# Kernel tuning notes

Measured on AMD Instinct MI355X. Metric: run time of the kernel, lower is better.

Reference implementation:

```python
import jax, jax.numpy as jnp
import numpy as np

B, T, C, H = 8, 1024, 1024, 16
Dh = C // H
EPS = 1e-5


def layernorm(x, g, b):
    m = jnp.mean(x, axis=-1, keepdims=True)
    v = jnp.mean((x - m) ** 2, axis=-1, keepdims=True)
    return g * (x - m) / jnp.sqrt(v + EPS) + b


def setup_inputs() -> dict:
    key = jax.random.key(0)
    ks = jax.random.split(key, 10)
    s = 0.02
    return {
        "x": jax.random.normal(ks[0], (B, T, C), jnp.float32),
        "Wq": jax.random.normal(ks[1], (H, C, Dh), jnp.float32) * s,
        "Wk": jax.random.normal(ks[2], (H, C, Dh), jnp.float32) * s,
        "Wv": jax.random.normal(ks[3], (H, C, Dh), jnp.float32) * s,
        "Wproj": jax.random.normal(ks[4], (C, C), jnp.float32) * s,
        "bproj": jnp.zeros((C,), jnp.float32),
        "W1": jax.random.normal(ks[5], (C, C), jnp.float32) * s,
        "b1": jnp.zeros((C,), jnp.float32),
        "W2": jax.random.normal(ks[6], (C, C), jnp.float32) * s,
        "b2": jnp.zeros((C,), jnp.float32),
        "g1": jnp.ones((C,), jnp.float32),
        "beta1": jnp.zeros((C,), jnp.float32),
        "g2": jnp.ones((C,), jnp.float32),
        "beta2": jnp.zeros((C,), jnp.float32),
    }


def reference(x, Wq, Wk, Wv, Wproj, bproj, W1, b1, W2, b2, g1, beta1, g2, beta2):
    # pre-LN multi-head causal self-attention + residual
    xn = layernorm(x, g1, beta1)
    q = jnp.einsum("btc,hcd->bhtd", xn, Wq)
    k = jnp.einsum("btc,hcd->bhtd", xn, Wk)
    v = jnp.einsum("btc,hcd->bhtd", xn, Wv)
    scores = jnp.einsum("bhtd,bhsd->bhts", q, k) * (Dh ** -0.5)
    causal = jnp.tril(jnp.ones((T, T), bool))  # [T,T]
    scores = jnp.where(causal, scores, -jnp.inf)
    wei = jax.nn.softmax(scores, axis=-1)
    attn = jnp.einsum("bhts,bhsd->bhtd", wei, v)
    attn = attn.transpose(0, 2, 1, 3).reshape(B, T, C)  # concat heads
    x = x + attn @ Wproj + bproj
    # pre-LN MLP (n_emb -> n_emb, ReLU, n_emb -> n_emb) + residual
    xn2 = layernorm(x, g2, beta2)
    h = jax.nn.relu(xn2 @ W1 + b1)
    x = x + h @ W2 + b2
    return x
```

## Files before the change

### kernel.cpp

```cpp
#include <hip/hip_runtime.h>
#include <hip/hip_bf16.h>

#define KDIM 1024

typedef __bf16  bf16x8  __attribute__((ext_vector_type(8)));
typedef float   floatx4 __attribute__((ext_vector_type(4)));

__device__ inline short f2bf(float f) {
    unsigned u = __float_as_uint(f);
    u += 0x7fffu + ((u >> 16) & 1u);
    return (short)(u >> 16);
}

__device__ inline floatx4 mfma16(bf16x8 a, bf16x8 b, floatx4 c) {
    return __builtin_amdgcn_mfma_f32_16x16x32_bf16(a, b, c, 0, 0, 0);
}

__device__ inline void load_lds16(const void* g, void* l) {
    __builtin_amdgcn_global_load_lds(
        (__attribute__((address_space(1))) void*)(unsigned long long)g,
        (__attribute__((address_space(3))) void*)(unsigned)(unsigned long long)l,
        16, 0, 0);
}

__global__ __launch_bounds__(256) void ln_kernel(
    const float* __restrict__ x, const float* __restrict__ g,
    const float* __restrict__ be, short* __restrict__ out)
{
    const int row = blockIdx.x, tid = threadIdx.x;
    const float4 v = ((const float4*)(x + (size_t)row * 1024))[tid];
    float s  = v.x + v.y + v.z + v.w;
    float s2 = v.x * v.x + v.y * v.y + v.z * v.z + v.w * v.w;
    #pragma unroll
    for (int off = 32; off; off >>= 1) {
        s  += __shfl_down(s, off);
        s2 += __shfl_down(s2, off);
    }
    __shared__ float red1[4], red2[4];
    const int w = tid >> 6, lane = tid & 63;
    if (lane == 0) { red1[w] = s; red2[w] = s2; }
    __syncthreads();
    s  = red1[0] + red1[1] + red1[2] + red1[3];
    s2 = red2[0] + red2[1] + red2[2] + red2[3];
    const float mean = s * (1.0f / 1024.0f);
    const float var  = s2 * (1.0f / 1024.0f) - mean * mean;
    const float rstd = rsqrtf(var + 1e-5f);
    const float4 gg = ((const float4*)g)[tid];
    const float4 bb = ((const float4*)be)[tid];
    short4 o;
    o.x = f2bf((v.x - mean) * rstd * gg.x + bb.x);
    o.y = f2bf((v.y - mean) * rstd * gg.y + bb.y);
    o.z = f2bf((v.z - mean) * rstd * gg.z + bb.z);
    o.w = f2bf((v.w - mean) * rstd * gg.w + bb.w);
    *(short4*)(out + (size_t)row * 1024 + tid * 4) = o;
}

__global__ void pack_qkvT(const float* __restrict__ Wq, const float* __restrict__ Wk,
                          const float* __restrict__ Wv, short* __restrict__ dst)
{
    __shared__ float tile[32][33];
    const int n0 = blockIdx.x * 32, c0 = blockIdx.y * 32;
    const int tx = threadIdx.x, ty = threadIdx.y;
    const int grp = n0 >> 10;
    const float* W = (grp == 0) ? Wq : (grp == 1 ? Wk : Wv);
    const int nb = n0 & 1023, hh = nb >> 6, d0 = nb & 63;
    #pragma unroll
    for (int j = 0; j < 32; j += 8)
        tile[ty + j][tx] = W[hh * 65536 + (c0 + ty + j) * 64 + d0 + tx];
    __syncthreads();
    #pragma unroll
    for (int j = 0; j < 32; j += 8)
        dst[(size_t)(n0 + ty + j) * 1024 + c0 + tx] = f2bf(tile[tx][ty + j]);
}

__global__ void packT(const float* __restrict__ src, short* __restrict__ dst)
{
    __shared__ float tile[32][33];
    const int n0 = blockIdx.x * 32, k0 = blockIdx.y * 32;
    const int tx = threadIdx.x, ty = threadIdx.y;
    #pragma unroll
    for (int j = 0; j < 32; j += 8)
        tile[ty + j][tx] = src[(size_t)(k0 + ty + j) * 1024 + n0 + tx];
    __syncthreads();
    #pragma unroll
    for (int j = 0; j < 32; j += 8)
        dst[(size_t)(n0 + ty + j) * 1024 + k0 + tx] = f2bf(tile[tx][ty + j]);
}

template <int EPI, bool SWAP>
__global__ __launch_bounds__(256) void gemm_bt(
    const short* __restrict__ A, const short* __restrict__ BT, int N,
    const float* __restrict__ bias, const float* __restrict__ resid,
    float* __restrict__ outF, short* __restrict__ outH,
    short* __restrict__ qO, short* __restrict__ kO, short* __restrict__ vtO)
{
    const int tid = threadIdx.x, lane = tid & 63, w = tid >> 6;
    const int wm = w >> 1, wn = w & 1;
    const int mi = lane & 15, quad = lane >> 4;
    const int rowBase = blockIdx.y * 128, colBase = blockIdx.x * 128;

    __shared__ alignas(16) short As[128 * 32];
    __shared__ alignas(16) short Bs[128 * 32];

    const floatx4 z4 = {0.f, 0.f, 0.f, 0.f};
    floatx4 acc[4][4];
    #pragma unroll
    for (int i = 0; i < 4; ++i)
        #pragma unroll
        for (int j = 0; j < 4; ++j) acc[i][j] = z4;

    for (int k0 = 0; k0 < KDIM; k0 += 32) {
        __syncthreads();
        #pragma unroll
        for (int i = 0; i < 2; ++i) {
            const int cb = i * 256 + w * 64;
            const int chunk = cb + lane;
            const int r = chunk >> 2, cc = chunk & 3;
            const int csw = cc ^ ((r >> 1) & 3);
            load_lds16(A  + (size_t)(rowBase + r) * KDIM + k0 + csw * 8, (char*)As + cb * 16);
            load_lds16(BT + (size_t)(colBase + r) * KDIM + k0 + csw * 8, (char*)Bs + cb * 16);
        }
        __syncthreads();
        bf16x8 af[4], bfv[4];
        #pragma unroll
        for (int it = 0; it < 4; ++it) {
            const int ra = wm * 64 + it * 16 + mi;
            af[it] = *(const bf16x8*)(As + ra * 32 + ((quad ^ ((ra >> 1) & 3)) << 3));
        }
        #pragma unroll
        for (int jt = 0; jt < 4; ++jt) {
            const int rb = wn * 64 + jt * 16 + mi;
            bfv[jt] = *(const bf16x8*)(Bs + rb * 32 + ((quad ^ ((rb >> 1) & 3)) << 3));
        }
        #pragma unroll
        for (int it = 0; it < 4; ++it)
            #pragma unroll
            for (int jt = 0; jt < 4; ++jt) {
                if constexpr (SWAP)
                    acc[it][jt] = mfma16(bfv[jt], af[it], acc[it][jt]);
                else
                    acc[it][jt] = mfma16(af[it], bfv[jt], acc[it][jt]);
            }
    }

    if constexpr (SWAP) {
        #pragma unroll
        for (int it = 0; it < 4; ++it) {
            const int row = rowBase + wm * 64 + it * 16 + mi;
            #pragma unroll
            for (int jt = 0; jt < 4; ++jt) {
                const int col0 = colBase + wn * 64 + jt * 16 + quad * 4;
                const floatx4 a4 = acc[it][jt];
                if constexpr (EPI == 0) {
                    if (colBase < 1024) {
                        short4 o;
                        o.x = f2bf(a4[0] * 0.125f); o.y = f2bf(a4[1] * 0.125f);
                        o.z = f2bf(a4[2] * 0.125f); o.w = f2bf(a4[3] * 0.125f);
                        *(short4*)(qO + (size_t)row * 1024 + col0) = o;
                    } else {
                        short4 o;
                        o.x = f2bf(a4[0]); o.y = f2bf(a4[1]);
                        o.z = f2bf(a4[2]); o.w = f2bf(a4[3]);
                        *(short4*)(kO + (size_t)row * 1024 + (col0 - 1024)) = o;
                    }
                } else if constexpr (EPI == 1) {
                    const float4 b4 = *(const float4*)(bias + col0);
                    const float4 r4 = *(const float4*)(resid + (size_t)row * N + col0);
                    float4 o;
                    o.x = a4[0] + b4.x + r4.x; o.y = a4[1] + b4.y + r4.y;
                    o.z = a4[2] + b4.z + r4.z; o.w = a4[3] + b4.w + r4.w;
                    *(float4*)(outF + (size_t)row * N + col0) = o;
                } else {
                    const float4 b4 = *(const float4*)(bias + col0);
                    short4 o;
                    o.x = f2bf(fmaxf(a4[0] + b4.x, 0.f));
                    o.y = f2bf(fmaxf(a4[1] + b4.y, 0.f));
                    o.z = f2bf(fmaxf(a4[2] + b4.z, 0.f));
                    o.w = f2bf(fmaxf(a4[3] + b4.w, 0.f));
                    *(short4*)(outH + (size_t)row * N + col0) = o;
                }
            }
        }
    } else {
        #pragma unroll
        for (int it = 0; it < 4; ++it) {
            const int row0 = rowBase + wm * 64 + it * 16 + quad * 4;
            const int bb = row0 >> 10, t0 = row0 & 1023;
            #pragma unroll
            for (int jt = 0; jt < 4; ++jt) {
                const int c = colBase + wn * 64 + jt * 16 + mi;
                const floatx4 a4 = acc[it][jt];
                short4 o;
                o.x = f2bf(a4[0]); o.y = f2bf(a4[1]);
                o.z = f2bf(a4[2]); o.w = f2bf(a4[3]);
                *(short4*)(vtO + ((size_t)bb << 20) + ((size_t)c << 10) + t0) = o;
            }
        }
    }
}

#define PSTR 88
__device__ __forceinline__ void attn_qk_pv(
    const bf16x8 qf0, const bf16x8 qf1,
    floatx4 (&o)[4], float (&lsum)[4],
    const short* Ks, const short* Vs, short* myP,
    const int mi, const int quad, const int kq, const int diagRowOff)
{
    const floatx4 z4 = {0.f, 0.f, 0.f, 0.f};
    const bool diag = diagRowOff >= 0;
    floatx4 sa[4];
    #pragma unroll
    for (int j = 0; j < 4; ++j) {
        const int row = j * 16 + mi;
        const int sw = row & 7;
        floatx4 s4 = z4;
        s4 = mfma16(qf0, *(const bf16x8*)(Ks + row * 64 + ((quad ^ sw) << 3)), s4);
        s4 = mfma16(qf1, *(const bf16x8*)(Ks + row * 64 + (((quad + 4) ^ sw) << 3)), s4);
        sa[j] = s4;
    }
    #pragma unroll
    for (int j = 0; j < 4; ++j)
        #pragma unroll
        for (int r = 0; r < 4; ++r) {
            float p = __expf(sa[j][r]);
            if (diag && (j * 16 + mi > diagRowOff + quad * 4 + r)) p = 0.f;
            lsum[r] += p;
            myP[(quad * 4 + r) * PSTR + j * 16 + mi] = f2bf(p);
        }
    __asm__ volatile("s_waitcnt lgkmcnt(0)" ::: "memory");
    const bf16x8 pf0 = *(const bf16x8*)(myP + mi * PSTR + kq);
    const bf16x8 pf1 = *(const bf16x8*)(myP + mi * PSTR + 32 + kq);
    #pragma unroll
    for (int d = 0; d < 4; ++d) {
        const int row = d * 16 + mi;
        const int sw = row & 7;
        o[d] = mfma16(pf0, *(const bf16x8*)(Vs + row * 64 + ((quad ^ sw) << 3)), o[d]);
        o[d] = mfma16(pf1, *(const bf16x8*)(Vs + row * 64 + (((quad + 4) ^ sw) << 3)), o[d]);
    }
}

__global__ __launch_bounds__(256, 4) void flash_attn(
    const short* __restrict__ Q, const short* __restrict__ K,
    const short* __restrict__ Vt, short* __restrict__ O)
{
    const int tid = threadIdx.x, lane = tid & 63, w = tid >> 6;
    const int mi = lane & 15, quad = lane >> 4, kq = quad * 8;
    const int pi = blockIdx.x;
    const int tA = pi, tB = 15 - pi;
    const int h = blockIdx.y, b = blockIdx.z;
    const int qbA = tA * 64, qbB = tB * 64;

    __shared__ alignas(16) short Ks[64 * 64];
    __shared__ alignas(16) short Vs[64 * 64];
    __shared__ alignas(16) short Ps[4][16 * PSTR];

    const size_t qoffA = ((size_t)(b * 1024 + qbA + w * 16 + mi)) * 1024 + h * 64;
    const size_t qoffB = ((size_t)(b * 1024 + qbB + w * 16 + mi)) * 1024 + h * 64;
    const bf16x8 qA0 = *(const bf16x8*)(Q + qoffA + kq);
    const bf16x8 qA1 = *(const bf16x8*)(Q + qoffA + 32 + kq);
    const bf16x8 qB0 = *(const bf16x8*)(Q + qoffB + kq);
    const bf16x8 qB1 = *(const bf16x8*)(Q + qoffB + 32 + kq);

    const floatx4 z4 = {0.f, 0.f, 0.f, 0.f};
    floatx4 oA[4], oB[4];
    float lA[4], lB[4];
    #pragma unroll
    for (int i = 0; i < 4; ++i) { oA[i] = z4; oB[i] = z4; lA[i] = 0.f; lB[i] = 0.f; }

    short* myP = &Ps[w][0];
    for (int t = 0; t <= tB; ++t) {
        const int s0 = t * 64;
        __syncthreads();
        #pragma unroll
        for (int i = 0; i < 2; ++i) {
            const int cb = i * 256 + w * 64;
            const int chunk = cb + lane;
            const int r = chunk >> 3, c = chunk & 7;
            const int csw = c ^ (r & 7);
            load_lds16(K + ((size_t)(b * 1024 + s0 + r)) * 1024 + h * 64 + csw * 8,
                       (char*)Ks + cb * 16);
            load_lds16(Vt + ((size_t)b << 20) + ((size_t)(h * 64 + r) << 10) + s0 + csw * 8,
                       (char*)Vs + cb * 16);
        }
        __syncthreads();

        if (t <= tA)
            attn_qk_pv(qA0, qA1, oA, lA, Ks, Vs, myP, mi, quad, kq,
                       (t == tA) ? (w * 16) : -1);
        attn_qk_pv(qB0, qB1, oB, lB, Ks, Vs, myP, mi, quad, kq,
                   (t == tB) ? (w * 16) : -1);
    }

    #pragma unroll
    for (int r = 0; r < 4; ++r) {
        float sA = lA[r], sB = lB[r];
        #pragma unroll
        for (int off = 1; off < 16; off <<= 1) {
            sA += __shfl_xor(sA, off);
            sB += __shfl_xor(sB, off);
        }
        lA[r] = 1.0f / sA;
        lB[r] = 1.0f / sB;
    }
    #pragma unroll
    for (int d = 0; d < 4; ++d)
        #pragma unroll
        for (int r = 0; r < 4; ++r) {
            const int col = h * 64 + d * 16 + mi;
            const int rowA = b * 1024 + qbA + w * 16 + quad * 4 + r;
            const int rowB = b * 1024 + qbB + w * 16 + quad * 4 + r;
            O[(size_t)rowA * 1024 + col] = f2bf(oA[d][r] * lA[r]);
            O[(size_t)rowB * 1024 + col] = f2bf(oB[d][r] * lB[r]);
        }
}

extern "C" void kernel_launch(void* const* d_in, const int* in_sizes, int n_in,
                              void* d_out, int out_size, void* d_ws, size_t ws_size,
                              hipStream_t stream)
{
    (void)in_sizes; (void)n_in; (void)out_size; (void)ws_size;
    const float* x     = (const float*)d_in[0];
    const float* Wq    = (const float*)d_in[1];
    const float* Wk    = (const float*)d_in[2];
    const float* Wv    = (const float*)d_in[3];
    const float* Wproj = (const float*)d_in[4];
    const float* bproj = (const float*)d_in[5];
    const float* W1    = (const float*)d_in[6];
    const float* b1    = (const float*)d_in[7];
    const float* W2    = (const float*)d_in[8];
    const float* b2    = (const float*)d_in[9];
    const float* g1    = (const float*)d_in[10];
    const float* be1   = (const float*)d_in[11];
    const float* g2    = (const float*)d_in[12];
    const float* be2   = (const float*)d_in[13];
    float* out = (float*)d_out;

    char* ws = (char*)d_ws;
    const size_t MB = 1u << 20;
    short* Qb     = (short*)(ws + 0 * MB);
    short* Kb     = (short*)(ws + 16 * MB);
    short* Vtb    = (short*)(ws + 32 * MB);
    short* XN     = (short*)(ws + 48 * MB);
    short* AT     = (short*)(ws + 64 * MB);
    float* R2     = (float*)(ws + 80 * MB);
    short* WqkvT  = (short*)(ws + 112 * MB);
    short* WprojT = (short*)(ws + 118 * MB);
    short* W1T    = (short*)(ws + 120 * MB);
    short* W2T    = (short*)(ws + 122 * MB);

    const dim3 tb(32, 8);
    pack_qkvT<<<dim3(96, 32), tb, 0, stream>>>(Wq, Wk, Wv, WqkvT);
    packT<<<dim3(32, 32), tb, 0, stream>>>(Wproj, WprojT);
    packT<<<dim3(32, 32), tb, 0, stream>>>(W1, W1T);
    packT<<<dim3(32, 32), tb, 0, stream>>>(W2, W2T);

    ln_kernel<<<8192, 256, 0, stream>>>(x, g1, be1, XN);

    gemm_bt<0, true><<<dim3(16, 64), 256, 0, stream>>>(XN, WqkvT, 1024,
        nullptr, nullptr, nullptr, nullptr, Qb, Kb, nullptr);
    gemm_bt<3, false><<<dim3(8, 64), 256, 0, stream>>>(XN, WqkvT + 2048 * KDIM, 1024,
        nullptr, nullptr, nullptr, nullptr, nullptr, nullptr, Vtb);

    flash_attn<<<dim3(8, 16, 8), 256, 0, stream>>>(Qb, Kb, Vtb, AT);

    gemm_bt<1, true><<<dim3(8, 64), 256, 0, stream>>>(AT, WprojT, 1024,
        bproj, x, R2, nullptr, nullptr, nullptr, nullptr);

    ln_kernel<<<8192, 256, 0, stream>>>(R2, g2, be2, XN);

    gemm_bt<2, true><<<dim3(8, 64), 256, 0, stream>>>(XN, W1T, 1024,
        b1, nullptr, nullptr, AT, nullptr, nullptr, nullptr);

    gemm_bt<1, true><<<dim3(8, 64), 256, 0, stream>>>(AT, W2T, 1024,
        b2, R2, out, nullptr, nullptr, nullptr, nullptr);
}
```

Before: 373.1 us.

## Deepen GEMM K-tile to 64, remap blocks per XCD, store residual in bf16

The GEMM main loop now stages 64-wide K slices with an 8-way XOR swizzle and runs two MFMA sub-steps per barrier pair, which halves the number of synchronisations. GEMM and flash-attention block indices are remapped so that neighbouring row tiles or heads land on the same XCD, aiming for better L2 reuse. The post-attention residual is written as bf16 instead of fp32, which cuts traffic for the second LayerNorm and the final residual add. The cost is doubled LDS per GEMM block and lower precision in the residual stream.

```diff
diff --git a/kernel.cpp b/kernel.cpp
--- a/kernel.cpp
+++ b/kernel.cpp
@@ -10,6 +10,9 @@
     unsigned u = __float_as_uint(f);
     u += 0x7fffu + ((u >> 16) & 1u);
     return (short)(u >> 16);
+}
+__device__ inline float bf2f(short s) {
+    return __uint_as_float(((unsigned)(unsigned short)s) << 16);
 }
 
 __device__ inline floatx4 mfma16(bf16x8 a, bf16x8 b, floatx4 c) {
@@ -23,12 +26,19 @@
         16, 0, 0);
 }
 
+template <bool BF16IN>
 __global__ __launch_bounds__(256) void ln_kernel(
-    const float* __restrict__ x, const float* __restrict__ g,
+    const void* __restrict__ xv, const float* __restrict__ g,
     const float* __restrict__ be, short* __restrict__ out)
 {
     const int row = blockIdx.x, tid = threadIdx.x;
-    const float4 v = ((const float4*)(x + (size_t)row * 1024))[tid];
+    float4 v;
+    if constexpr (BF16IN) {
+        const short4 s4 = ((const short4*)xv)[(size_t)row * 256 + tid];
+        v.x = bf2f(s4.x); v.y = bf2f(s4.y); v.z = bf2f(s4.z); v.w = bf2f(s4.w);
+    } else {
+        v = ((const float4*)xv)[(size_t)row * 256 + tid];
+    }
     float s  = v.x + v.y + v.z + v.w;
     float s2 = v.x * v.x + v.y * v.y + v.z * v.z + v.w * v.w;
     #pragma unroll
@@ -90,17 +100,21 @@
 template <int EPI, bool SWAP>
 __global__ __launch_bounds__(256) void gemm_bt(
     const short* __restrict__ A, const short* __restrict__ BT, int N,
-    const float* __restrict__ bias, const float* __restrict__ resid,
+    const float* __restrict__ bias, const float* __restrict__ residF,
+    const short* __restrict__ residH,
     float* __restrict__ outF, short* __restrict__ outH,
     short* __restrict__ qO, short* __restrict__ kO, short* __restrict__ vtO)
 {
     const int tid = threadIdx.x, lane = tid & 63, w = tid >> 6;
     const int wm = w >> 1, wn = w & 1;
     const int mi = lane & 15, quad = lane >> 4;
-    const int rowBase = blockIdx.y * 128, colBase = blockIdx.x * 128;
-
-    __shared__ alignas(16) short As[128 * 32];
-    __shared__ alignas(16) short Bs[128 * 32];
+    const int lid = blockIdx.x + gridDim.x * blockIdx.y;
+    const int xcd = lid & 7, i8 = lid >> 3;
+    const int rowBase = (xcd * 8 + (i8 & 7)) * 128;
+    const int colBase = (i8 >> 3) * 128;
+
+    __shared__ alignas(16) short As[128 * 64];
+    __shared__ alignas(16) short Bs[128 * 64];
 
     const floatx4 z4 = {0.f, 0.f, 0.f, 0.f};
     floatx4 acc[4][4];
@@ -109,38 +123,41 @@
         #pragma unroll
         for (int j = 0; j < 4; ++j) acc[i][j] = z4;
 
-    for (int k0 = 0; k0 < KDIM; k0 += 32) {
+    for (int k0 = 0; k0 < KDIM; k0 += 64) {
         __syncthreads();
         #pragma unroll
-        for (int i = 0; i < 2; ++i) {
+        for (int i = 0; i < 4; ++i) {
             const int cb = i * 256 + w * 64;
             const int chunk = cb + lane;
-            const int r = chunk >> 2, cc = chunk & 3;
-            const int csw = cc ^ ((r >> 1) & 3);
+            const int r = chunk >> 3, c = chunk & 7;
+            const int csw = c ^ (r & 7);
             load_lds16(A  + (size_t)(rowBase + r) * KDIM + k0 + csw * 8, (char*)As + cb * 16);
             load_lds16(BT + (size_t)(colBase + r) * KDIM + k0 + csw * 8, (char*)Bs + cb * 16);
         }
         __syncthreads();
-        bf16x8 af[4], bfv[4];
-        #pragma unroll
-        for (int it = 0; it < 4; ++it) {
-            const int ra = wm * 64 + it * 16 + mi;
-            af[it] = *(const bf16x8*)(As + ra * 32 + ((quad ^ ((ra >> 1) & 3)) << 3));
-        }
-        #pragma unroll
-        for (int jt = 0; jt < 4; ++jt) {
-            const int rb = wn * 64 + jt * 16 + mi;
-            bfv[jt] = *(const bf16x8*)(Bs + rb * 32 + ((quad ^ ((rb >> 1) & 3)) << 3));
-        }
-        #pragma unroll
-        for (int it = 0; it < 4; ++it)
+        #pragma unroll
+        for (int kh = 0; kh < 2; ++kh) {
+            bf16x8 af[4], bfv[4];
+            #pragma unroll
+            for (int it = 0; it < 4; ++it) {
+                const int ra = wm * 64 + it * 16 + mi;
+                af[it] = *(const bf16x8*)(As + (ra * 8 + ((kh * 4 + quad) ^ (ra & 7))) * 8);
+            }
             #pragma unroll
             for (int jt = 0; jt < 4; ++jt) {
-                if constexpr (SWAP)
-                    acc[it][jt] = mfma16(bfv[jt], af[it], acc[it][jt]);
-                else
-                    acc[it][jt] = mfma16(af[it], bfv[jt], acc[it][jt]);
+                const int rb = wn * 64 + jt * 16 + mi;
+                bfv[jt] = *(const bf16x8*)(Bs + (rb * 8 + ((kh * 4 + quad) ^ (rb & 7))) * 8);
             }
+            #pragma unroll
+            for (int it = 0; it < 4; ++it)
+                #pragma unroll
+                for (int jt = 0; jt < 4; ++jt) {
+                    if constexpr (SWAP)
+                        acc[it][jt] = mfma16(bfv[jt], af[it], acc[it][jt]);
+                    else
+                        acc[it][jt] = mfma16(af[it], bfv[jt], acc[it][jt]);
+                }
+        }
     }
 
     if constexpr (SWAP) {
@@ -163,14 +180,7 @@
                         o.z = f2bf(a4[2]); o.w = f2bf(a4[3]);
                         *(short4*)(kO + (size_t)row * 1024 + (col0 - 1024)) = o;
                     }
-                } else if constexpr (EPI == 1) {
-                    const float4 b4 = *(const float4*)(bias + col0);
-                    const float4 r4 = *(const float4*)(resid + (size_t)row * N + col0);
-                    float4 o;
-                    o.x = a4[0] + b4.x + r4.x; o.y = a4[1] + b4.y + r4.y;
-                    o.z = a4[2] + b4.z + r4.z; o.w = a4[3] + b4.w + r4.w;
-                    *(float4*)(outF + (size_t)row * N + col0) = o;
-                } else {
+                } else if constexpr (EPI == 2) {
                     const float4 b4 = *(const float4*)(bias + col0);
                     short4 o;
                     o.x = f2bf(fmaxf(a4[0] + b4.x, 0.f));
@@ -178,6 +188,24 @@
                     o.z = f2bf(fmaxf(a4[2] + b4.z, 0.f));
                     o.w = f2bf(fmaxf(a4[3] + b4.w, 0.f));
                     *(short4*)(outH + (size_t)row * N + col0) = o;
+                } else if constexpr (EPI == 4) {
+                    const float4 b4 = *(const float4*)(bias + col0);
+                    const float4 r4 = *(const float4*)(residF + (size_t)row * N + col0);
+                    short4 o;
+                    o.x = f2bf(a4[0] + b4.x + r4.x);
+                    o.y = f2bf(a4[1] + b4.y + r4.y);
+                    o.z = f2bf(a4[2] + b4.z + r4.z);
+                    o.w = f2bf(a4[3] + b4.w + r4.w);
+                    *(short4*)(outH + (size_t)row * N + col0) = o;
+                } else {
+                    const float4 b4 = *(const float4*)(bias + col0);
+                    const short4 r4 = *(const short4*)(residH + (size_t)row * N + col0);
+                    float4 o;
+                    o.x = a4[0] + b4.x + bf2f(r4.x);
+                    o.y = a4[1] + b4.y + bf2f(r4.y);
+                    o.z = a4[2] + b4.z + bf2f(r4.z);
+                    o.w = a4[3] + b4.w + bf2f(r4.w);
+                    *(float4*)(outF + (size_t)row * N + col0) = o;
                 }
             }
         }
@@ -245,9 +273,12 @@
 {
     const int tid = threadIdx.x, lane = tid & 63, w = tid >> 6;
     const int mi = lane & 15, quad = lane >> 4, kq = quad * 8;
-    const int pi = blockIdx.x;
+    const int lid = blockIdx.x;
+    const int xcd = lid & 7, i8 = lid >> 3;
+    const int bh = xcd * 16 + (i8 & 15);
+    const int pi = i8 >> 4;
+    const int h = bh & 15, b = bh >> 4;
     const int tA = pi, tB = 15 - pi;
-    const int h = blockIdx.y, b = blockIdx.z;
     const int qbA = tA * 64, qbB = tB * 64;
 
     __shared__ alignas(16) short Ks[64 * 64];
@@ -342,7 +373,7 @@
     short* Vtb    = (short*)(ws + 32 * MB);
     short* XN     = (short*)(ws + 48 * MB);
     short* AT     = (short*)(ws + 64 * MB);
-    float* R2     = (float*)(ws + 80 * MB);
+    short* R2b    = (short*)(ws + 80 * MB);
     short* WqkvT  = (short*)(ws + 112 * MB);
     short* WprojT = (short*)(ws + 118 * MB);
     short* W1T    = (short*)(ws + 120 * MB);
@@ -354,23 +385,23 @@
     packT<<<dim3(32, 32), tb, 0, stream>>>(W1, W1T);
     packT<<<dim3(32, 32), tb, 0, stream>>>(W2, W2T);
 
-    ln_kernel<<<8192, 256, 0, stream>>>(x, g1, be1, XN);
+    ln_kernel<false><<<8192, 256, 0, stream>>>(x, g1, be1, XN);
 
     gemm_bt<0, true><<<dim3(16, 64), 256, 0, stream>>>(XN, WqkvT, 1024,
-        nullptr, nullptr, nullptr, nullptr, Qb, Kb, nullptr);
+        nullptr, nullptr, nullptr, nullptr, nullptr, Qb, Kb, nullptr);
     gemm_bt<3, false><<<dim3(8, 64), 256, 0, stream>>>(XN, WqkvT + 2048 * KDIM, 1024,
-        nullptr, nullptr, nullptr, nullptr, nullptr, nullptr, Vtb);
-
-    flash_attn<<<dim3(8, 16, 8), 256, 0, stream>>>(Qb, Kb, Vtb, AT);
-
-    gemm_bt<1, true><<<dim3(8, 64), 256, 0, stream>>>(AT, WprojT, 1024,
-        bproj, x, R2, nullptr, nullptr, nullptr, nullptr);
-
-    ln_kernel<<<8192, 256, 0, stream>>>(R2, g2, be2, XN);
+        nullptr, nullptr, nullptr, nullptr, nullptr, nullptr, nullptr, Vtb);
+
+    flash_attn<<<1024, 256, 0, stream>>>(Qb, Kb, Vtb, AT);
+
+    gemm_bt<4, true><<<dim3(8, 64), 256, 0, stream>>>(AT, WprojT, 1024,
+        bproj, x, nullptr, nullptr, R2b, nullptr, nullptr, nullptr);
+
+    ln_kernel<true><<<8192, 256, 0, stream>>>(R2b, g2, be2, XN);
 
     gemm_bt<2, true><<<dim3(8, 64), 256, 0, stream>>>(XN, W1T, 1024,
-        b1, nullptr, nullptr, AT, nullptr, nullptr, nullptr);
-
-    gemm_bt<1, true><<<dim3(8, 64), 256, 0, stream>>>(AT, W2T, 1024,
-        b2, R2, out, nullptr, nullptr, nullptr, nullptr);
-}
+        b1, nullptr, nullptr, nullptr, AT, nullptr, nullptr, nullptr);
+
+    gemm_bt<5, true><<<dim3(8, 64), 256, 0, stream>>>(AT, W2T, 1024,
+        b2, nullptr, R2b, out, nullptr, nullptr, nullptr, nullptr);
+}
```

Result: faster. 326.7 us (-12.4%).
